# Optimization experiments

Hardware: AMD Instinct MI355X
Metric: run time of the kernel (lower is better)

Reference implementation:

```python
import jax, jax.numpy as jnp
import numpy as np

N, E, HDIM, EDIM, MSG_H, UPD_H = 50000, 640000, 128, 32, 128, 128
LN_EPS = 1e-5


def setup_inputs() -> dict:
    key = jax.random.key(0)
    ks = jax.random.split(key, 12)
    def lin(k, fan_in, fan_out):
        return jax.random.normal(k, (fan_in, fan_out), dtype=jnp.float32) / np.sqrt(fan_in)
    h = jax.random.normal(ks[0], (N, HDIM), dtype=jnp.float32)
    edge_index = jax.random.randint(ks[1], (2, E), 0, N, dtype=jnp.int32)
    edge_attr = jax.random.normal(ks[2], (E, EDIM), dtype=jnp.float32)
    return {
        "h": h,
        "edge_index": edge_index,
        "edge_attr": edge_attr,
        # edge MLP: Linear(2*hdim+edim -> msg_hidden), ReLU, Linear(msg_hidden -> hdim)
        "ew1": lin(ks[3], 2 * HDIM + EDIM, MSG_H),
        "eb1": jnp.zeros((MSG_H,), jnp.float32),
        "ew2": lin(ks[4], MSG_H, HDIM),
        "eb2": jnp.zeros((HDIM,), jnp.float32),
        # node MLP: Linear(2*hdim -> upd_hidden), ReLU, Linear(upd_hidden -> hdim)
        "nw1": lin(ks[5], 2 * HDIM, UPD_H),
        "nb1": jnp.zeros((UPD_H,), jnp.float32),
        "nw2": lin(ks[6], UPD_H, HDIM),
        "nb2": jnp.zeros((HDIM,), jnp.float32),
        # LayerNorm(hdim)
        "gamma": jnp.ones((HDIM,), jnp.float32),
        "beta": jnp.zeros((HDIM,), jnp.float32),
    }


def reference(h, edge_index, edge_attr, ew1, eb1, ew2, eb2, nw1, nb1, nw2, nb2, gamma, beta):
    src, dst = edge_index[0], edge_index[1]
    # gather + concat -> edge MLP  (eval mode: dropout inactive, edge_dropout off)
    m_in = jnp.concatenate([h[src], h[dst], edge_attr], axis=1)       # [E, 2H+EDIM]
    m = jax.nn.relu(m_in @ ew1 + eb1) @ ew2 + eb2                     # [E, H]
    # scatter-add messages into destination nodes
    agg = jax.ops.segment_sum(m, dst, num_segments=h.shape[0])        # [N, H]
    # node update MLP
    u_in = jnp.concatenate([h, agg], axis=1)                          # [N, 2H]
    h_upd = jax.nn.relu(u_in @ nw1 + nb1) @ nw2 + nb2                 # [N, H]
    # residual + LayerNorm
    x = h + h_upd
    mu = jnp.mean(x, axis=-1, keepdims=True)
    var = jnp.mean(jnp.square(x - mu), axis=-1, keepdims=True)
    return (x - mu) * jax.lax.rsqrt(var + LN_EPS) * gamma + beta
```

## Files before the change

kernel.cpp:

```cpp
#include <hip/hip_runtime.h>
#include <cstdint>

#define HD 128
#define ED 32
#define BME 64
#define BMN 128
#define PAD_N 264
#define PAD_T 136
#define EGRID 512

typedef _Float16 f16;
typedef __attribute__((ext_vector_type(2))) _Float16 f16x2;
typedef __attribute__((ext_vector_type(4))) _Float16 f16x4;
typedef __attribute__((ext_vector_type(8))) _Float16 f16x8;
typedef __attribute__((ext_vector_type(4))) float    f32x4;
typedef __attribute__((ext_vector_type(4))) unsigned int u32x4;

__device__ __forceinline__ f32x4 mfma16(f16x8 a, f16x8 b, f32x4 c) {
    return __builtin_amdgcn_mfma_f32_16x16x32_f16(a, b, c, 0, 0, 0);
}
__device__ __forceinline__ f16x8 cvt8(const float* p) {
    const float4 a0 = *(const float4*)p;
    const float4 a1 = *(const float4*)(p + 4);
    f16x8 v;
    v[0] = (f16)a0.x; v[1] = (f16)a0.y; v[2] = (f16)a0.z; v[3] = (f16)a0.w;
    v[4] = (f16)a1.x; v[5] = (f16)a1.y; v[6] = (f16)a1.z; v[7] = (f16)a1.w;
    return v;
}

__global__ __launch_bounds__(256) void zero_f32(float4* p, long n4) {
    long i = (long)blockIdx.x * blockDim.x + threadIdx.x;
    const long stride = (long)gridDim.x * blockDim.x;
    const float4 z = make_float4(0.f, 0.f, 0.f, 0.f);
    for (; i < n4; i += stride) p[i] = z;
}
__global__ __launch_bounds__(256) void zero_i32(int* p, int n) {
    int i = blockIdx.x * blockDim.x + threadIdx.x;
    if (i < n) p[i] = 0;
}
__global__ __launch_bounds__(256)
void cvt_f16_kernel(const float* __restrict__ x, f16* __restrict__ y, long n8) {
    long i = blockIdx.x * 256 + threadIdx.x;
    const long stride = (long)gridDim.x * 256;
    for (; i < n8; i += stride) *(f16x8*)(y + i * 8) = cvt8(x + i * 8);
}
__global__ __launch_bounds__(256)
void pack_all_kernel(const float* __restrict__ ew1, const float* __restrict__ ew2,
                     const float* __restrict__ nw1, const float* __restrict__ nw2,
                     f16* __restrict__ w1p, f16* __restrict__ w2p,
                     f16* __restrict__ n1p, f16* __restrict__ n2p)
{
    const int b = blockIdx.x;
    const float* w; f16* wp; int base;
    if (b < 18)      { w = ew1; wp = w1p; base = b; }
    else if (b < 26) { w = ew2; wp = w2p; base = b - 18; }
    else if (b < 42) { w = nw1; wp = n1p; base = b - 26; }
    else             { w = nw2; wp = n2p; base = b - 42; }
    const int idx = base * 256 + threadIdx.x;
    const int l  = idx & 63;
    const int fr = idx >> 6;
    const int wi = fr & 7, kt = fr >> 3;
    const int lii = l & 15, qq = l >> 4;
    const float* p = w + (size_t)(32 * kt + 8 * qq) * HD + 16 * wi + lii;
    f16x8 v;
#pragma unroll
    for (int e2 = 0; e2 < 8; ++e2) v[e2] = (f16)p[(size_t)e2 * HD];
    *(f16x8*)(wp + (size_t)idx * 8) = v;
}

__global__ __launch_bounds__(256)
void hist_kernel(const int* __restrict__ eidx, int* __restrict__ rank,
                 int* __restrict__ cnt, int E) {
    int e = blockIdx.x * 256 + threadIdx.x;
    if (e < E) rank[e] = atomicAdd(&cnt[eidx[E + e]], 1);
}
__global__ __launch_bounds__(1024)
void scan_kernel(const int* __restrict__ cnt, int* __restrict__ rs, int N) {
    __shared__ int wsum[16];
    __shared__ int s_carry;
    const int t = threadIdx.x, lane = t & 63, wid = t >> 6;
    if (t == 0) s_carry = 0;
    __syncthreads();
    for (int base = 0; base < N; base += 1024) {
        const int i = base + t;
        const int v = (i < N) ? cnt[i] : 0;
        int incl = v;
#pragma unroll
        for (int off = 1; off < 64; off <<= 1) {
            int u = __shfl_up(incl, off, 64);
            if (lane >= off) incl += u;
        }
        if (lane == 63) wsum[wid] = incl;
        __syncthreads();
        if (t == 0) {
            int s = 0;
#pragma unroll
            for (int w = 0; w < 16; ++w) { int x = wsum[w]; wsum[w] = s; s += x; }
        }
        __syncthreads();
        const int carry = s_carry;
        if (i < N) rs[i] = carry + wsum[wid] + incl - v;
        __syncthreads();
        if (t == 1023) s_carry = carry + wsum[15] + incl;
        __syncthreads();
    }
    if (threadIdx.x == 0) rs[N] = s_carry;
}
__global__ __launch_bounds__(256)
void pos_kernel(const int* __restrict__ eidx, const int* __restrict__ rs,
                int* __restrict__ pos, int E) {
    int e = blockIdx.x * 256 + threadIdx.x;
    if (e < E) pos[e] = rs[eidx[E + e]] + pos[e];
}

template <int MODE>
__global__ __launch_bounds__(512, 4)
void edge_kernel(const f16*   __restrict__ h16,
                 const int*   __restrict__ eidx,
                 const float* __restrict__ ea,
                 const f16*   __restrict__ w1p,
                 const float* __restrict__ b1,
                 const f16*   __restrict__ w2p,
                 const float* __restrict__ b2,
                 void*        __restrict__ aggm,
                 const int*   __restrict__ pos,
                 int E, int ntiles)
{
    __shared__ __align__(16) f16 sA[BME * 320];
    __shared__ __align__(16) f16 sT[BME * 128];
    __shared__ int sIdx[2][BME];

    const int t  = threadIdx.x;
    const int l  = t & 63;
    const int wv = t >> 6;
    const int li = l & 15;
    const int q  = l >> 4;
    const int lm = l & 7;
    const int r  = t >> 3;
    const int q8 = t & 7;

    f16x8 A1[9], A2[4];
#pragma unroll
    for (int kt = 0; kt < 9; ++kt)
        A1[kt] = *(const f16x8*)(w1p + ((size_t)(kt * 8 + wv) * 64 + l) * 8);
#pragma unroll
    for (int kt = 0; kt < 4; ++kt)
        A2[kt] = *(const f16x8*)(w2p + ((size_t)(kt * 8 + wv) * 64 + l) * 8);

    f16x8 d[4];
    f16x8 d4;
    int   psr = 0;
    auto prefetch = [&](int tile) {
        const int ec  = min(tile * BME + r, E - 1);
        const int src = eidx[ec];
        const int dst = eidx[E + ec];
        psr = (MODE == 0) ? dst : pos[ec];
        const f16* hs = h16 + (size_t)src * HD;
        const f16* hd = h16 + (size_t)dst * HD;
#pragma unroll
        for (int i = 0; i < 4; ++i) {
            const int c = (q8 + 8 * i) * 8;
            d[i] = (c < HD) ? *(const f16x8*)(hs + c)
                            : *(const f16x8*)(hd + (c - HD));
        }
        if (q8 < 4) d4 = cvt8(ea + (size_t)ec * ED + q8 * 8);
    };

    int tb = blockIdx.x;
    if (tb < ntiles) prefetch(tb);
    int par = 0;

    for (; tb < ntiles; tb += gridDim.x, par ^= 1) {
        {
            f16* row = sA + r * 320;
            const int sw = r & 7;
#pragma unroll
            for (int i = 0; i < 4; ++i) {
                const int ch = q8 + 8 * i;
                *(f16x8*)(row + ((ch ^ sw) * 8)) = d[i];
            }
            if (q8 < 4)
                *(f16x8*)(row + (((q8 + 32) ^ sw) * 8)) = d4;
            if (q8 == 0) sIdx[par][r] = psr;
        }
        __syncthreads();

        const int nt = tb + (int)gridDim.x;
        if (nt < ntiles) prefetch(nt);

        f32x4 acc[4];
#pragma unroll
        for (int j = 0; j < 4; ++j) acc[j] = (f32x4){0.f, 0.f, 0.f, 0.f};
#pragma unroll
        for (int kt = 0; kt < 9; ++kt) {
#pragma unroll
            for (int et = 0; et < 4; ++et) {
                const f16x8 b = *(const f16x8*)(sA + (16 * et + li) * 320
                                                + (((4 * kt + q) ^ lm) * 8));
                acc[et] = mfma16(A1[kt], b, acc[et]);
            }
        }

        {
            const int hidb = 16 * wv + 4 * q;
            const float4 bb = *(const float4*)(b1 + hidb);
            const int chT = hidb >> 3;
            const int off = hidb & 7;
#pragma unroll
            for (int et = 0; et < 4; ++et) {
                const f32x4 v = acc[et];
                float x0 = fmaxf(v[0] + bb.x, 0.f), x1 = fmaxf(v[1] + bb.y, 0.f);
                float x2 = fmaxf(v[2] + bb.z, 0.f), x3 = fmaxf(v[3] + bb.w, 0.f);
                f16x4 o; o[0] = (f16)x0; o[1] = (f16)x1; o[2] = (f16)x2; o[3] = (f16)x3;
                *(f16x4*)(sT + (16 * et + li) * 128 + ((chT ^ lm) * 8) + off) = o;
            }
        }
        __syncthreads();

        f32x4 acc2[4];
#pragma unroll
        for (int j = 0; j < 4; ++j) acc2[j] = (f32x4){0.f, 0.f, 0.f, 0.f};
#pragma unroll
        for (int kt = 0; kt < 4; ++kt) {
#pragma unroll
            for (int et = 0; et < 4; ++et) {
                const f16x8 b = *(const f16x8*)(sT + (16 * et + li) * 128
                                                + (((4 * kt + q) ^ lm) * 8));
                acc2[et] = mfma16(A2[kt], b, acc2[et]);
            }
        }

        if (MODE == 0) {
            float* agg = (float*)aggm;
            const int hidb = 16 * wv + 4 * q;
            const float4 bb = *(const float4*)(b2 + hidb);
#pragma unroll
            for (int et = 0; et < 4; ++et) {
                const int edge = 16 * et + li;
                if (tb * BME + edge < E) {
                    float* p = agg + (size_t)sIdx[par][edge] * HD + hidb;
                    const f32x4 v = acc2[et];
                    atomicAdd(p + 0, v[0] + bb.x);
                    atomicAdd(p + 1, v[1] + bb.y);
                    atomicAdd(p + 2, v[2] + bb.z);
                    atomicAdd(p + 3, v[3] + bb.w);
                }
            }
            __syncthreads();
        } else {
            __syncthreads();
            {
                const int hidb = 16 * wv + 4 * q;
                const float4 bb = *(const float4*)(b2 + hidb);
                const int chT = hidb >> 3;
                const int off = hidb & 7;
#pragma unroll
                for (int et = 0; et < 4; ++et) {
                    const f32x4 v = acc2[et];
                    f16x4 o;
                    o[0] = (f16)(v[0] + bb.x); o[1] = (f16)(v[1] + bb.y);
                    o[2] = (f16)(v[2] + bb.z); o[3] = (f16)(v[3] + bb.w);
                    *(f16x4*)(sT + (16 * et + li) * 128 + ((chT ^ lm) * 8) + off) = o;
                }
            }
            __syncthreads();
            f16* m = (f16*)aggm;
#pragma unroll
            for (int i = 0; i < 2; ++i) {
                const int idx  = t + i * 512;
                const int row2 = idx >> 4;
                const int c    = idx & 15;
                if (tb * BME + row2 < E) {
                    const f16x8 v = *(const f16x8*)(sT + row2 * 128
                                                    + ((c ^ (row2 & 7)) * 8));
                    __builtin_nontemporal_store(*(const u32x4*)&v,
                        (u32x4*)(m + (size_t)sIdx[par][row2] * HD + c * 8));
                }
            }
        }
    }
}

__global__ __launch_bounds__(256)
void gather_kernel(const f16* __restrict__ m, const int* __restrict__ rs,
                   f16* __restrict__ aggb, int N)
{
    const int n = blockIdx.x * 4 + (threadIdx.x >> 6);
    if (n >= N) return;
    const int lane = threadIdx.x & 63;
    const int s = rs[n], e = rs[n + 1];
    const f16* base = m + (size_t)s * HD + lane * 2;
    const int cnt = e - s;
    float a0 = 0.f, b0 = 0.f, a1 = 0.f, b1 = 0.f;
    int j = 0;
    for (; j + 2 <= cnt; j += 2) {
        const unsigned int uu = __builtin_nontemporal_load(
            (const unsigned int*)(base + (size_t)j * HD));
        const unsigned int vv = __builtin_nontemporal_load(
            (const unsigned int*)(base + (size_t)(j + 1) * HD));
        const f16x2 u = *(const f16x2*)&uu;
        const f16x2 v = *(const f16x2*)&vv;
        a0 += (float)u[0]; b0 += (float)u[1];
        a1 += (float)v[0]; b1 += (float)v[1];
    }
    if (j < cnt) {
        const unsigned int uu = __builtin_nontemporal_load(
            (const unsigned int*)(base + (size_t)j * HD));
        const f16x2 u = *(const f16x2*)&uu;
        a0 += (float)u[0]; b0 += (float)u[1];
    }
    f16x2 rr; rr[0] = (f16)(a0 + a1); rr[1] = (f16)(b0 + b1);
    *(f16x2*)(aggb + (size_t)n * HD + lane * 2) = rr;
}

template <int CSR>
__global__ __launch_bounds__(256, 2)
void node_kernel(const f16*   __restrict__ h16,
                 const float* __restrict__ h,
                 const f16*   __restrict__ aggb,
                 const float* __restrict__ aggf,
                 const f16*   __restrict__ w1p,
                 const float* __restrict__ b1,
                 const f16*   __restrict__ w2p,
                 const float* __restrict__ b2,
                 const float* __restrict__ gamma,
                 const float* __restrict__ beta,
                 float*       __restrict__ out,
                 int N)
{
    __shared__ __align__(16) f16 sA[BMN * PAD_N];
    __shared__ float sMV[2 * BMN];

    const int t  = threadIdx.x;
    const int l  = t & 63;
    const int wv = t >> 6;
    const int li = l & 15;
    const int q  = l >> 4;
    const int nbase = blockIdx.x * BMN;

    {
        const int r = t >> 1, half = t & 1;
        const int node = min(nbase + r, N - 1);
        f16* rowp = sA + r * PAD_N + half * HD;
        if (half == 0) {
            const f16* src = h16 + (size_t)node * HD;
#pragma unroll
            for (int i = 0; i < 16; ++i)
                *(f16x8*)(rowp + i * 8) = *(const f16x8*)(src + i * 8);
        } else if (CSR) {
            const f16* src = aggb + (size_t)node * HD;
#pragma unroll
            for (int i = 0; i < 16; ++i)
                *(f16x8*)(rowp + i * 8) = *(const f16x8*)(src + i * 8);
        } else {
            const float* src = aggf + (size_t)node * HD;
#pragma unroll
            for (int i = 0; i < 16; ++i)
                *(f16x8*)(rowp + i * 8) = cvt8(src + i * 8);
        }
    }

    f16x8 A1[2][8];
#pragma unroll
    for (int ht = 0; ht < 2; ++ht)
#pragma unroll
        for (int kt = 0; kt < 8; ++kt)
            A1[ht][kt] = *(const f16x8*)(w1p + ((size_t)(kt * 8 + wv * 2 + ht) * 64 + l) * 8);
    __syncthreads();

    f32x4 acc[2][8];
#pragma unroll
    for (int i = 0; i < 2; ++i)
#pragma unroll
        for (int j = 0; j < 8; ++j) acc[i][j] = (f32x4){0.f, 0.f, 0.f, 0.f};
#pragma unroll
    for (int kt = 0; kt < 8; ++kt) {
#pragma unroll
        for (int et = 0; et < 8; ++et) {
            const f16x8 b = *(const f16x8*)(sA + (16 * et + li) * PAD_N + 32 * kt + 8 * q);
            acc[0][et] = mfma16(A1[0][kt], b, acc[0][et]);
            acc[1][et] = mfma16(A1[1][kt], b, acc[1][et]);
        }
    }
    __syncthreads();

    f16x8 A2[2][4];
#pragma unroll
    for (int ht = 0; ht < 2; ++ht)
#pragma unroll
        for (int kt = 0; kt < 4; ++kt)
            A2[ht][kt] = *(const f16x8*)(w2p + ((size_t)(kt * 8 + wv * 2 + ht) * 64 + l) * 8);

    f16* sT = sA;
#pragma unroll
    for (int ht = 0; ht < 2; ++ht) {
        const int hidb = 32 * wv + 16 * ht + 4 * q;
        const float4 bb = *(const float4*)(b1 + hidb);
#pragma unroll
        for (int et = 0; et < 8; ++et) {
            const f32x4 v = acc[ht][et];
            float x0 = fmaxf(v[0] + bb.x, 0.f), x1 = fmaxf(v[1] + bb.y, 0.f);
            float x2 = fmaxf(v[2] + bb.z, 0.f), x3 = fmaxf(v[3] + bb.w, 0.f);
            f16x4 o; o[0] = (f16)x0; o[1] = (f16)x1; o[2] = (f16)x2; o[3] = (f16)x3;
            *(f16x4*)(sT + (16 * et + li) * PAD_T + hidb) = o;
        }
    }
    __syncthreads();

    f32x4 acc2[2][8];
#pragma unroll
    for (int i = 0; i < 2; ++i)
#pragma unroll
        for (int j = 0; j < 8; ++j) acc2[i][j] = (f32x4){0.f, 0.f, 0.f, 0.f};
#pragma unroll
    for (int kt = 0; kt < 4; ++kt) {
#pragma unroll
        for (int et = 0; et < 8; ++et) {
            const f16x8 b = *(const f16x8*)(sT + (16 * et + li) * PAD_T + 32 * kt + 8 * q);
            acc2[0][et] = mfma16(A2[0][kt], b, acc2[0][et]);
            acc2[1][et] = mfma16(A2[1][kt], b, acc2[1][et]);
        }
    }
    __syncthreads();

    float* sX = (float*)sA;
#pragma unroll
    for (int ht = 0; ht < 2; ++ht) {
        const int hidb = 32 * wv + 16 * ht + 4 * q;
        const float4 bb = *(const float4*)(b2 + hidb);
#pragma unroll
        for (int et = 0; et < 8; ++et) {
            const int node = 16 * et + li;
            const int nc   = min(nbase + node, N - 1);
            const float4 hv = *(const float4*)(h + (size_t)nc * HD + hidb);
            const f32x4 v = acc2[ht][et];
            f32x4 x;
            x[0] = v[0] + bb.x + hv.x;
            x[1] = v[1] + bb.y + hv.y;
            x[2] = v[2] + bb.z + hv.z;
            x[3] = v[3] + bb.w + hv.w;
            *(f32x4*)(sX + (size_t)node * 132 + hidb) = x;
        }
    }
    __syncthreads();

    {
        const int node  = t >> 1;
        const int half2 = t & 1;
        const float* px = sX + node * 132 + half2 * 64;
        float s = 0.f, sq = 0.f;
#pragma unroll
        for (int i = 0; i < 16; ++i) {
            const float4 v = *(const float4*)(px + i * 4);
            s  += v.x + v.y + v.z + v.w;
            sq += v.x * v.x + v.y * v.y + v.z * v.z + v.w * v.w;
        }
        s  += __shfl_xor(s, 1);
        sq += __shfl_xor(sq, 1);
        if (!half2) {
            const float mean = s * (1.f / HD);
            const float var  = sq * (1.f / HD) - mean * mean;
            sMV[node]       = mean;
            sMV[BMN + node] = rsqrtf(var + 1e-5f);
        }
    }
    __syncthreads();

#pragma unroll
    for (int i = 0; i < 16; ++i) {
        const int idx  = t + i * 256;
        const int node = idx >> 5;
        const int c4   = (idx & 31) * 4;
        if (nbase + node < N) {
            const float4 xv = *(const float4*)(sX + node * 132 + c4);
            const float4 g4 = *(const float4*)(gamma + c4);
            const float4 b4 = *(const float4*)(beta + c4);
            const float mean = sMV[node];
            const float rstd = sMV[BMN + node];
            float4 o;
            o.x = (xv.x - mean) * rstd * g4.x + b4.x;
            o.y = (xv.y - mean) * rstd * g4.y + b4.y;
            o.z = (xv.z - mean) * rstd * g4.z + b4.z;
            o.w = (xv.w - mean) * rstd * g4.w + b4.w;
            *(float4*)(out + (size_t)(nbase + node) * HD + c4) = o;
        }
    }
}

extern "C" void kernel_launch(void* const* d_in, const int* in_sizes, int n_in,
                              void* d_out, int out_size, void* d_ws, size_t ws_size,
                              hipStream_t stream)
{
    const float* h     = (const float*)d_in[0];
    const int*   eidx  = (const int*)  d_in[1];
    const float* ea    = (const float*)d_in[2];
    const float* ew1   = (const float*)d_in[3];
    const float* eb1   = (const float*)d_in[4];
    const float* ew2   = (const float*)d_in[5];
    const float* eb2   = (const float*)d_in[6];
    const float* nw1   = (const float*)d_in[7];
    const float* nb1   = (const float*)d_in[8];
    const float* nw2   = (const float*)d_in[9];
    const float* nb2   = (const float*)d_in[10];
    const float* gamma = (const float*)d_in[11];
    const float* beta  = (const float*)d_in[12];
    float* out = (float*)d_out;

    const int N = in_sizes[0] / HD;
    const int E = in_sizes[1] / 2;
    const int ntiles = (E + BME - 1) / BME;

    size_t off = 0;
    auto alloc = [&](size_t bytes) {
        size_t o = off; off += (bytes + 255) & ~(size_t)255; return o;
    };
    const size_t o_m    = alloc((size_t)E * HD * sizeof(f16));
    const size_t o_agb  = alloc((size_t)N * HD * sizeof(f16));
    const size_t o_h16  = alloc((size_t)N * HD * sizeof(f16));
    const size_t o_pos  = alloc((size_t)E * sizeof(int));
    const size_t o_rs   = alloc((size_t)(N + 1) * sizeof(int));
    const size_t o_cnt  = alloc((size_t)N * sizeof(int));
    const size_t o_w1p  = alloc((size_t)9 * 8 * 64 * 8 * sizeof(f16));
    const size_t o_w2p  = alloc((size_t)4 * 8 * 64 * 8 * sizeof(f16));
    const size_t o_n1p  = alloc((size_t)8 * 8 * 64 * 8 * sizeof(f16));
    const size_t o_n2p  = alloc((size_t)4 * 8 * 64 * 8 * sizeof(f16));
    const bool csr = (off <= ws_size);
    char* ws = (char*)d_ws;

    if (csr) {
        f16* mb   = (f16*)(ws + o_m);
        f16* aggb = (f16*)(ws + o_agb);
        f16* h16  = (f16*)(ws + o_h16);
        int* pos  = (int*)(ws + o_pos);
        int* rs   = (int*)(ws + o_rs);
        int* cnt  = (int*)(ws + o_cnt);
        f16* w1p  = (f16*)(ws + o_w1p);
        f16* w2p  = (f16*)(ws + o_w2p);
        f16* n1p  = (f16*)(ws + o_n1p);
        f16* n2p  = (f16*)(ws + o_n2p);

        zero_i32<<<(N + 255) / 256, 256, 0, stream>>>(cnt, N);
        hist_kernel<<<(E + 255) / 256, 256, 0, stream>>>(eidx, pos, cnt, E);
        scan_kernel<<<1, 1024, 0, stream>>>(cnt, rs, N);
        pos_kernel<<<(E + 255) / 256, 256, 0, stream>>>(eidx, rs, pos, E);
        cvt_f16_kernel<<<2048, 256, 0, stream>>>(h, h16, (long)N * HD / 8);
        pack_all_kernel<<<50, 256, 0, stream>>>(ew1, ew2, nw1, nw2, w1p, w2p, n1p, n2p);
        edge_kernel<1><<<EGRID, 512, 0, stream>>>(
            h16, eidx, ea, w1p, eb1, w2p, eb2, (void*)mb, pos, E, ntiles);
        gather_kernel<<<(N + 3) / 4, 256, 0, stream>>>(mb, rs, aggb, N);
        node_kernel<1><<<(N + BMN - 1) / BMN, 256, 0, stream>>>(
            h16, h, aggb, nullptr, n1p, nb1, n2p, nb2, gamma, beta, out, N);
    } else {
        size_t foff = 0;
        auto falloc = [&](size_t bytes) {
            size_t o = foff; foff += (bytes + 255) & ~(size_t)255; return o;
        };
        float* agg = (float*)(ws + falloc((size_t)N * HD * sizeof(float)));
        f16*   h16 = (f16*)  (ws + falloc((size_t)N * HD * sizeof(f16)));
        f16*   w1p = (f16*)  (ws + falloc((size_t)9 * 8 * 64 * 8 * sizeof(f16)));
        f16*   w2p = (f16*)  (ws + falloc((size_t)4 * 8 * 64 * 8 * sizeof(f16)));
        f16*   n1p = (f16*)  (ws + falloc((size_t)8 * 8 * 64 * 8 * sizeof(f16)));
        f16*   n2p = (f16*)  (ws + falloc((size_t)4 * 8 * 64 * 8 * sizeof(f16)));

        zero_f32<<<1024, 256, 0, stream>>>((float4*)agg, (long)N * HD / 4);
        cvt_f16_kernel<<<2048, 256, 0, stream>>>(h, h16, (long)N * HD / 8);
        pack_all_kernel<<<50, 256, 0, stream>>>(ew1, ew2, nw1, nw2, w1p, w2p, n1p, n2p);
        edge_kernel<0><<<EGRID, 512, 0, stream>>>(
            h16, eidx, ea, w1p, eb1, w2p, eb2, (void*)agg, nullptr, E, ntiles);
        node_kernel<0><<<(N + BMN - 1) / BMN, 256, 0, stream>>>(
            h16, h, nullptr, agg, n1p, nb1, n2p, nb2, gamma, beta, out, N);
    }
}
```

Baseline: 281.7 us.

## Fuse CSR message gather into node kernel and use lighter LDS barriers

Removes the separate gather kernel and makes the node kernel sum each node's incoming messages directly from the CSR-sorted message buffer into shared memory. This saves a kernel launch and the write and re-read of the aggregated f16 buffer. In exchange, each node is now reduced by only two threads with 64 float accumulators each, which raises register pressure and lowers memory parallelism compared with the 64-lane-per-node gather. The edge kernel's __syncthreads are also replaced with an explicit lgkmcnt wait plus s_barrier.

```diff
diff --git a/kernel.cpp b/kernel.cpp
--- a/kernel.cpp
+++ b/kernel.cpp
@@ -26,6 +26,11 @@
     v[0] = (f16)a0.x; v[1] = (f16)a0.y; v[2] = (f16)a0.z; v[3] = (f16)a0.w;
     v[4] = (f16)a1.x; v[5] = (f16)a1.y; v[6] = (f16)a1.z; v[7] = (f16)a1.w;
     return v;
+}
+__device__ __forceinline__ void barrier_lds() {
+    asm volatile("s_waitcnt lgkmcnt(0)" ::: "memory");
+    __builtin_amdgcn_s_barrier();
+    __builtin_amdgcn_sched_barrier(0);
 }
 
 __global__ __launch_bounds__(256) void zero_f32(float4* p, long n4) {
@@ -183,7 +188,7 @@
                 *(f16x8*)(row + (((q8 + 32) ^ sw) * 8)) = d4;
             if (q8 == 0) sIdx[par][r] = psr;
         }
-        __syncthreads();
+        barrier_lds();
 
         const int nt = tb + (int)gridDim.x;
         if (nt < ntiles) prefetch(nt);
@@ -215,7 +220,7 @@
                 *(f16x4*)(sT + (16 * et + li) * 128 + ((chT ^ lm) * 8) + off) = o;
             }
         }
-        __syncthreads();
+        barrier_lds();
 
         f32x4 acc2[4];
 #pragma unroll
@@ -246,9 +251,9 @@
                     atomicAdd(p + 3, v[3] + bb.w);
                 }
             }
-            __syncthreads();
+            barrier_lds();
         } else {
-            __syncthreads();
+            barrier_lds();
             {
                 const int hidb = 16 * wv + 4 * q;
                 const float4 bb = *(const float4*)(b2 + hidb);
@@ -263,7 +268,7 @@
                     *(f16x4*)(sT + (16 * et + li) * 128 + ((chT ^ lm) * 8) + off) = o;
                 }
             }
-            __syncthreads();
+            barrier_lds();
             f16* m = (f16*)aggm;
 #pragma unroll
             for (int i = 0; i < 2; ++i) {
@@ -281,43 +286,12 @@
     }
 }
 
-__global__ __launch_bounds__(256)
-void gather_kernel(const f16* __restrict__ m, const int* __restrict__ rs,
-                   f16* __restrict__ aggb, int N)
-{
-    const int n = blockIdx.x * 4 + (threadIdx.x >> 6);
-    if (n >= N) return;
-    const int lane = threadIdx.x & 63;
-    const int s = rs[n], e = rs[n + 1];
-    const f16* base = m + (size_t)s * HD + lane * 2;
-    const int cnt = e - s;
-    float a0 = 0.f, b0 = 0.f, a1 = 0.f, b1 = 0.f;
-    int j = 0;
-    for (; j + 2 <= cnt; j += 2) {
-        const unsigned int uu = __builtin_nontemporal_load(
-            (const unsigned int*)(base + (size_t)j * HD));
-        const unsigned int vv = __builtin_nontemporal_load(
-            (const unsigned int*)(base + (size_t)(j + 1) * HD));
-        const f16x2 u = *(const f16x2*)&uu;
-        const f16x2 v = *(const f16x2*)&vv;
-        a0 += (float)u[0]; b0 += (float)u[1];
-        a1 += (float)v[0]; b1 += (float)v[1];
-    }
-    if (j < cnt) {
-        const unsigned int uu = __builtin_nontemporal_load(
-            (const unsigned int*)(base + (size_t)j * HD));
-        const f16x2 u = *(const f16x2*)&uu;
-        a0 += (float)u[0]; b0 += (float)u[1];
-    }
-    f16x2 rr; rr[0] = (f16)(a0 + a1); rr[1] = (f16)(b0 + b1);
-    *(f16x2*)(aggb + (size_t)n * HD + lane * 2) = rr;
-}
-
 template <int CSR>
 __global__ __launch_bounds__(256, 2)
 void node_kernel(const f16*   __restrict__ h16,
                  const float* __restrict__ h,
-                 const f16*   __restrict__ aggb,
+                 const f16*   __restrict__ m,
+                 const int*   __restrict__ rs,
                  const float* __restrict__ aggf,
                  const f16*   __restrict__ w1p,
                  const float* __restrict__ b1,
@@ -341,24 +315,43 @@
     {
         const int r = t >> 1, half = t & 1;
         const int node = min(nbase + r, N - 1);
-        f16* rowp = sA + r * PAD_N + half * HD;
-        if (half == 0) {
-            const f16* src = h16 + (size_t)node * HD;
-#pragma unroll
-            for (int i = 0; i < 16; ++i)
-                *(f16x8*)(rowp + i * 8) = *(const f16x8*)(src + i * 8);
-        } else if (CSR) {
-            const f16* src = aggb + (size_t)node * HD;
-#pragma unroll
-            for (int i = 0; i < 16; ++i)
-                *(f16x8*)(rowp + i * 8) = *(const f16x8*)(src + i * 8);
+        f16* rowp = sA + r * PAD_N;
+        {
+            const f16* srcp = h16 + (size_t)node * HD + half * 64;
+#pragma unroll
+            for (int i = 0; i < 8; ++i)
+                *(f16x8*)(rowp + half * 64 + i * 8) = *(const f16x8*)(srcp + i * 8);
+        }
+        if (CSR) {
+            const int s = rs[node], en = rs[node + 1];
+            float ag[64];
+#pragma unroll
+            for (int i = 0; i < 64; ++i) ag[i] = 0.f;
+            const f16* base = m + (size_t)s * HD + half * 64;
+            for (int j = 0; j < en - s; ++j) {
+                const f16* rp = base + (size_t)j * HD;
+#pragma unroll
+                for (int i = 0; i < 8; ++i) {
+                    const f16x8 v = *(const f16x8*)(rp + i * 8);
+#pragma unroll
+                    for (int k2 = 0; k2 < 8; ++k2) ag[i * 8 + k2] += (float)v[k2];
+                }
+            }
+#pragma unroll
+            for (int i = 0; i < 8; ++i) {
+                f16x8 o;
+#pragma unroll
+                for (int k2 = 0; k2 < 8; ++k2) o[k2] = (f16)ag[i * 8 + k2];
+                *(f16x8*)(rowp + 128 + half * 64 + i * 8) = o;
+            }
         } else {
-            const float* src = aggf + (size_t)node * HD;
-#pragma unroll
-            for (int i = 0; i < 16; ++i)
-                *(f16x8*)(rowp + i * 8) = cvt8(src + i * 8);
-        }
-    }
+            const float* srcp = aggf + (size_t)node * HD + half * 64;
+#pragma unroll
+            for (int i = 0; i < 8; ++i)
+                *(f16x8*)(rowp + 128 + half * 64 + i * 8) = cvt8(srcp + i * 8);
+        }
+    }
+    __syncthreads();
 
     f16x8 A1[2][8];
 #pragma unroll
@@ -366,7 +359,6 @@
 #pragma unroll
         for (int kt = 0; kt < 8; ++kt)
             A1[ht][kt] = *(const f16x8*)(w1p + ((size_t)(kt * 8 + wv * 2 + ht) * 64 + l) * 8);
-    __syncthreads();
 
     f32x4 acc[2][8];
 #pragma unroll
@@ -515,7 +507,6 @@
         size_t o = off; off += (bytes + 255) & ~(size_t)255; return o;
     };
     const size_t o_m    = alloc((size_t)E * HD * sizeof(f16));
-    const size_t o_agb  = alloc((size_t)N * HD * sizeof(f16));
     const size_t o_h16  = alloc((size_t)N * HD * sizeof(f16));
     const size_t o_pos  = alloc((size_t)E * sizeof(int));
     const size_t o_rs   = alloc((size_t)(N + 1) * sizeof(int));
@@ -529,7 +520,6 @@
 
     if (csr) {
         f16* mb   = (f16*)(ws + o_m);
-        f16* aggb = (f16*)(ws + o_agb);
         f16* h16  = (f16*)(ws + o_h16);
         int* pos  = (int*)(ws + o_pos);
         int* rs   = (int*)(ws + o_rs);
@@ -547,9 +537,8 @@
         pack_all_kernel<<<50, 256, 0, stream>>>(ew1, ew2, nw1, nw2, w1p, w2p, n1p, n2p);
         edge_kernel<1><<<EGRID, 512, 0, stream>>>(
             h16, eidx, ea, w1p, eb1, w2p, eb2, (void*)mb, pos, E, ntiles);
-        gather_kernel<<<(N + 3) / 4, 256, 0, stream>>>(mb, rs, aggb, N);
         node_kernel<1><<<(N + BMN - 1) / BMN, 256, 0, stream>>>(
-            h16, h, aggb, nullptr, n1p, nb1, n2p, nb2, gamma, beta, out, N);
+            h16, h, mb, rs, nullptr, n1p, nb1, n2p, nb2, gamma, beta, out, N);
     } else {
         size_t foff = 0;
         auto falloc = [&](size_t bytes) {
@@ -568,6 +557,6 @@
         edge_kernel<0><<<EGRID, 512, 0, stream>>>(
             h16, eidx, ea, w1p, eb1, w2p, eb2, (void*)agg, nullptr, E, ntiles);
         node_kernel<0><<<(N + BMN - 1) / BMN, 256, 0, stream>>>(
-            h16, h, nullptr, agg, n1p, nb1, n2p, nb2, gamma, beta, out, N);
-    }
-}
+            h16, h, nullptr, nullptr, agg, n1p, nb1, n2p, nb2, gamma, beta, out, N);
+    }
+}
```

New measurement: 281.4 us. No clear change (-0.1%).
